# Kernel optimization log

Measured on AMD Instinct MI355X. Metric: run time of the kernel, lower is better.

## Reference

```python
import jax, jax.numpy as jnp
import numpy as np

HID = 256  # LSTM hidden size (hard-coded in Renet)


def _lstm_dir(x, wih, whh, b):
    # x: [N, T, D]; PyTorch LSTM gate order: i, f, g, o
    def cell(carry, xt):
        h, c = carry
        g = xt @ wih.T + h @ whh.T + b
        i, f, gg, o = jnp.split(g, 4, axis=-1)
        c = jax.nn.sigmoid(f) * c + jax.nn.sigmoid(i) * jnp.tanh(gg)
        h = jax.nn.sigmoid(o) * jnp.tanh(c)
        return (h, c), h
    n = x.shape[0]
    h0 = jnp.zeros((n, HID), x.dtype)
    _, hs = jax.lax.scan(cell, (h0, h0), jnp.swapaxes(x, 0, 1))
    return jnp.swapaxes(hs, 0, 1)  # [N, T, HID]


def _bilstm(x, wf, uf, bf, wb, ub, bb):
    hf = _lstm_dir(x, wf, uf, bf)
    hb = _lstm_dir(x[:, ::-1], wb, ub, bb)[:, ::-1]
    return jnp.concatenate([hf, hb], axis=-1)  # [N, T, 2*HID]


def setup_inputs() -> dict:
    key = jax.random.key(0)
    ks = jax.random.split(key, 16)
    B, C, S = 8, 512, 64
    def p(k, shape):
        return 0.05 * jax.random.normal(k, shape, jnp.float32)
    d = {}
    d['x'] = jax.random.normal(ks[0], (B, C, S, S), jnp.float32)
    d['v_wih_f'] = p(ks[1], (4 * HID, C))
    d['v_whh_f'] = p(ks[2], (4 * HID, HID))
    d['v_b_f'] = p(ks[3], (4 * HID,))
    d['v_wih_b'] = p(ks[4], (4 * HID, C))
    d['v_whh_b'] = p(ks[5], (4 * HID, HID))
    d['v_b_b'] = p(ks[6], (4 * HID,))
    d['h_wih_f'] = p(ks[7], (4 * HID, 2 * HID))
    d['h_whh_f'] = p(ks[8], (4 * HID, HID))
    d['h_b_f'] = p(ks[9], (4 * HID,))
    d['h_wih_b'] = p(ks[10], (4 * HID, 2 * HID))
    d['h_whh_b'] = p(ks[11], (4 * HID, HID))
    d['h_b_b'] = p(ks[12], (4 * HID,))
    d['conv_w'] = p(ks[13], (22 * 22, 2 * HID))
    d['conv_b'] = p(ks[14], (22 * 22,))
    return d


def reference(x, v_wih_f, v_whh_f, v_b_f, v_wih_b, v_whh_b, v_b_b,
              h_wih_f, h_whh_f, h_b_f, h_wih_b, h_whh_b, h_b_b,
              conv_w, conv_b):
    B, C, H, W = x.shape
    # ---- Renet ----
    xt = jnp.transpose(x, (0, 2, 3, 1))  # [B,H,W,C]
    # vertical LSTM: sequence along W, batched over all B*H rows at once
    v = _bilstm(xt.reshape(B * H, W, C), v_wih_f, v_whh_f, v_b_f,
                v_wih_b, v_whh_b, v_b_b).reshape(B, H, W, 2 * HID)
    # horizontal LSTM: sequence along H, batched over all B*W columns
    h = _bilstm(jnp.transpose(v, (0, 2, 1, 3)).reshape(B * W, H, 2 * HID),
                h_wih_f, h_whh_f, h_b_f, h_wih_b, h_whh_b,
                h_b_b).reshape(B, W, H, 2 * HID)
    feat = jnp.transpose(h, (0, 3, 2, 1))  # [B, 512, H, W]
    kern = jnp.einsum('bchw,oc->bohw', feat, conv_w) + conv_b[None, :, None, None]
    # ---- PicanetG ----
    kern = jax.nn.softmax(kern, axis=1)  # softmax over 484 channel dim
    # unfold(k=22, dilation=3) with H=W=64 yields exactly one global dilated patch
    patch = x[:, :, ::3, ::3].reshape(B, C, 22 * 22)  # [B, C, 484]
    out = jnp.einsum('bck,bkl->bcl', patch, kern.reshape(B, 22 * 22, H * W))
    return out.reshape(B, C, H, W)
```

## Files before the change

kernel.cpp:

```cpp
#include <hip/hip_runtime.h>
#include <hip/hip_bf16.h>
#include <hip/hip_fp8.h>
#include <math.h>


typedef __hip_bfloat16 bf16;
typedef short short8 __attribute__((ext_vector_type(8)));
typedef float f4 __attribute__((ext_vector_type(4)));
typedef int int4v __attribute__((ext_vector_type(4)));
typedef int int8v __attribute__((ext_vector_type(8)));

#define SCL8 0x7F7F7F7F

__device__ __forceinline__ unsigned short bfbits(float f) {
    bf16 h = __float2bfloat16(f);
    return *reinterpret_cast<unsigned short*>(&h);
}
__device__ __forceinline__ float bf2f(unsigned short u) {
    union { unsigned int i; float f; } x; x.i = ((unsigned int)u) << 16; return x.f;
}
__device__ __forceinline__ unsigned char f2fp8(float f) {
    __hip_fp8_e4m3 q(f);
    return *reinterpret_cast<unsigned char*>(&q);
}
__device__ __forceinline__ float sigm2(float x) {
    return __builtin_amdgcn_rcpf(1.0f + __builtin_amdgcn_exp2f(x * -1.44269504f));
}
__device__ __forceinline__ float tanh2(float x) {
    return 1.0f - 2.0f * __builtin_amdgcn_rcpf(1.0f + __builtin_amdgcn_exp2f(x * 2.88539008f));
}

#define GLD16(g, s) __builtin_amdgcn_global_load_lds(                          \
    (const __attribute__((address_space(1))) void*)(g),                        \
    (__attribute__((address_space(3))) void*)(s), 16, 0, 0)

#define LGKM_BARRIER() do {                                                    \
    asm volatile("s_waitcnt lgkmcnt(0)" ::: "memory");                         \
    __builtin_amdgcn_s_barrier();                                              \
} while (0)

__global__ __launch_bounds__(256)
void prep_weights(const float* __restrict__ w0, const float* __restrict__ w1,
                  const float* __restrict__ w2, const float* __restrict__ w3,
                  const float* __restrict__ cw, const float* __restrict__ cb,
                  const float* __restrict__ u0, const float* __restrict__ u1,
                  const float* __restrict__ u2, const float* __restrict__ u3,
                  bf16* __restrict__ wt, bf16* __restrict__ cw2b,
                  float* __restrict__ cb2, unsigned char* __restrict__ wq)
{
    int idx = blockIdx.x * 256 + threadIdx.x;
    if (idx < 2097152) {
        int mat = idx >> 19, rem = idx & 524287;
        const float* src = (mat == 0) ? w0 : (mat == 1) ? w1 : (mat == 2) ? w2 : w3;
        wt[idx] = __float2bfloat16(src[rem]);
    } else if (idx < 2097152 + 262144) {
        int r = idx - 2097152; int o = r >> 9, k = r & 511;
        cw2b[r] = __float2bfloat16((o < 484) ? cw[o * 512 + k] : 0.f);
    } else if (idx < 2097152 + 262144 + 512) {
        int o = idx - 2097152 - 262144;
        cb2[o] = (o < 484) ? cb[o] : 0.f;
    } else if (idx < 2097152 + 262144 + 512 + 1048576) {
        int r = idx - 2097152 - 262144 - 512;
        int mat = r >> 18, rem = r & 262143;
        const float* src = (mat == 0) ? u0 : (mat == 1) ? u1 : (mat == 2) ? u2 : u3;
        wq[r] = f2fp8(src[rem]);
    }
}

__global__ __launch_bounds__(256)
void xtrans(const float* __restrict__ x, bf16* __restrict__ xt)
{
    __shared__ float T[64][65];
    const int tid = threadIdx.x;
    const int bid = blockIdx.x;
    const int b = bid >> 9, h = (bid >> 3) & 63, ct = bid & 7;
    const int c0 = ct << 6;
    const float* xp = x + ((long)(b * 512 + c0) * 64 + h) * 64;
    const int wv = tid >> 6, wl = tid & 63;
    #pragma unroll
    for (int r = 0; r < 16; ++r) {
        int ci = wv + (r << 2);
        T[ci][wl] = xp[(long)ci * 4096 + wl];
    }
    __syncthreads();
    const int wr = tid >> 2, cj = (tid & 3) << 4;
    bf16* op = xt + ((long)(b * 4096 + h * 64 + wr) * 512) + c0 + cj;
    short8 v0, v1;
    #pragma unroll
    for (int i = 0; i < 8; ++i) v0[i] = (short)bfbits(T[cj + i][wr]);
    #pragma unroll
    for (int i = 0; i < 8; ++i) v1[i] = (short)bfbits(T[cj + 8 + i][wr]);
    *(short8*)op = v0;
    *(short8*)(op + 8) = v1;
}

template<int MODE>
__global__ __launch_bounds__(256)
void gemm_lds(const bf16* __restrict__ A, const bf16* __restrict__ W,
              const float* __restrict__ biasf, const float* __restrict__ biasb,
              void* __restrict__ outf, void* __restrict__ outb, int dironly)
{
    __shared__ alignas(16) char Abuf[16384];
    __shared__ alignas(16) char Bbuf[16384];
    const int tid = threadIdx.x;
    const int wv = tid >> 6, l = tid & 63;
    const int lm = l & 15, lg = l >> 4;
    const int wm = wv >> 1, wn = wv & 1;

    const int nx = gridDim.x;
    int bid = blockIdx.y * nx + blockIdx.x;
    const int cpx = (nx * gridDim.y) >> 3;
    bid = (bid & 7) * cpx + (bid >> 3);
    const int bx = bid % nx;
    const int n0 = (bid / nx) << 7;

    int dir = 0, jblk = 0, g0 = 0;
    const bf16* Wg = W;
    if (MODE == 0) {
        dir  = (dironly < 0) ? (bx >> 3) : dironly;
        jblk = (dironly < 0) ? (bx & 7) : bx;
    } else {
        g0 = bx << 7;
        if (MODE == 2) Wg += (long)(n0 >> 9) * 2097152;
    }

    f4 acc[4][4];
    #pragma unroll
    for (int mf = 0; mf < 4; ++mf)
        #pragma unroll
        for (int nf = 0; nf < 4; ++nf)
            acc[mf][nf] = (f4){0.f, 0.f, 0.f, 0.f};

    for (int kt = 0; kt < 8; ++kt) {
        const int k0 = kt << 6;
        #pragma unroll
        for (int i = 0; i < 4; ++i) {
            const int seg = (wv << 2) + i;
            const int L = (seg << 10) + l * 16;
            const int row = L >> 7;
            const int off = (L & 127) ^ ((row & 7) << 4);
            const bf16* ga = A + (long)(n0 + row) * 512 + k0 + (off >> 1);
            GLD16(ga, &Abuf[seg << 10]);
        }
        #pragma unroll
        for (int i = 0; i < 4; ++i) {
            const int seg = (wv << 2) + i;
            const int L = (seg << 10) + l * 16;
            const int row = L >> 7;
            const int off = (L & 127) ^ ((row & 7) << 4);
            int wrow;
            if (MODE == 0) wrow = (dir << 10) + ((row >> 5) << 8) + jblk * 32 + (row & 31);
            else           wrow = g0 + row;
            const bf16* gb = Wg + (long)wrow * 512 + k0 + (off >> 1);
            GLD16(gb, &Bbuf[seg << 10]);
        }
        __syncthreads();

        #pragma unroll
        for (int kk = 0; kk < 2; ++kk) {
            short8 af[4], bq[4];
            #pragma unroll
            for (int mf = 0; mf < 4; ++mf) {
                const int row = wm * 64 + mf * 16 + lm;
                const int ad = (row << 7) + ((((kk << 6) + (lg << 4))) ^ ((row & 7) << 4));
                af[mf] = *(const short8*)&Abuf[ad];
            }
            #pragma unroll
            for (int nf = 0; nf < 4; ++nf) {
                const int row = (MODE == 0) ? (nf * 32 + wn * 16 + lm)
                                            : (wn * 64 + nf * 16 + lm);
                const int ad = (row << 7) + ((((kk << 6) + (lg << 4))) ^ ((row & 7) << 4));
                bq[nf] = *(const short8*)&Bbuf[ad];
            }
            #pragma unroll
            for (int mf = 0; mf < 4; ++mf)
                #pragma unroll
                for (int nf = 0; nf < 4; ++nf)
                    acc[mf][nf] = __builtin_amdgcn_mfma_f32_16x16x32_bf16(af[mf], bq[nf], acc[mf][nf], 0, 0, 0);
        }
        __syncthreads();
    }

    if (MODE == 0) {
        const float* bs = dir ? biasb : biasf;
        const int jglob = jblk * 32 + wn * 16 + lm;
        float bv[4];
        #pragma unroll
        for (int nf = 0; nf < 4; ++nf) bv[nf] = bs[nf * 256 + jglob];
        ushort4* Gd = (ushort4*)(dir ? outb : outf);
        #pragma unroll
        for (int mf = 0; mf < 4; ++mf) {
            #pragma unroll
            for (int r = 0; r < 4; ++r) {
                const int n = n0 + wm * 64 + mf * 16 + lg * 4 + r;
                ushort4 u;
                u.x = bfbits(acc[mf][0][r] + bv[0]);
                u.y = bfbits(acc[mf][1][r] + bv[1]);
                u.z = bfbits(acc[mf][2][r] + bv[2]);
                u.w = bfbits(acc[mf][3][r] + bv[3]);
                Gd[(long)n * 256 + jglob] = u;
            }
        }
    } else if (MODE == 1) {
        float bv[4];
        #pragma unroll
        for (int nf = 0; nf < 4; ++nf) bv[nf] = biasf[g0 + wn * 64 + nf * 16 + lm];
        float* o = (float*)outf;
        #pragma unroll
        for (int mf = 0; mf < 4; ++mf)
            #pragma unroll
            for (int r = 0; r < 4; ++r) {
                const int n = n0 + wm * 64 + mf * 16 + lg * 4 + r;
                #pragma unroll
                for (int nf = 0; nf < 4; ++nf)
                    o[(long)n * 512 + g0 + wn * 64 + nf * 16 + lm] = acc[mf][nf][r] + bv[nf];
            }
    } else {
        float* o = (float*)outf;
        #pragma unroll
        for (int mf = 0; mf < 4; ++mf)
            #pragma unroll
            for (int r = 0; r < 4; ++r) {
                const int n = n0 + wm * 64 + mf * 16 + lg * 4 + r;
                #pragma unroll
                for (int nf = 0; nf < 4; ++nf)
                    o[(long)n * 4096 + g0 + wn * 64 + nf * 16 + lm] = acc[mf][nf][r];
            }
    }
}

__global__ __launch_bounds__(1024, 4)
void lstm4s(const bf16* __restrict__ Gf, const bf16* __restrict__ Gb,
            const unsigned char* __restrict__ Wqf, const unsigned char* __restrict__ Wqb,
            bf16* __restrict__ Out, int dir_force)
{
    __shared__ char ldspad[83968];
    __shared__ unsigned char hbuf[2][4][256];
    const int tid = threadIdx.x;
    const int wv = tid >> 6, l = tid & 63;
    const int lm = l & 15, lg = l >> 4;
    const int j_c = wv * 16 + lm;
    const int s_a = lm >> 2;

    int dir, sblk;
    if (dir_force >= 0) { dir = dir_force; sblk = blockIdx.x; }
    else               { dir = blockIdx.x >> 7; sblk = blockIdx.x & 127; }
    if (dir_force == -9999) ((volatile char*)ldspad)[tid] = 1;

    const bf16* G = dir ? Gb : Gf;
    const unsigned char* WQ = dir ? Wqb : Wqf;
    const int s0 = sblk << 2;

    int8v wfrag[4][2];
    #pragma unroll
    for (int q = 0; q < 4; ++q) {
        const unsigned char* wr = WQ + (long)(q * 256 + wv * 16 + lm) * 256 + lg * 32;
        #pragma unroll
        for (int kt = 0; kt < 2; ++kt) {
            int4v lo = *(const int4v*)(wr + kt * 128);
            int4v hi = *(const int4v*)(wr + kt * 128 + 16);
            int8v w;
            w[0] = lo[0]; w[1] = lo[1]; w[2] = lo[2]; w[3] = lo[3];
            w[4] = hi[0]; w[5] = hi[1]; w[6] = hi[2]; w[7] = hi[3];
            wfrag[q][kt] = w;
        }
    }

    if (tid < 256) ((unsigned long*)hbuf)[tid] = 0ul;

    float cst = 0.f;
    const ushort4* G4 = (const ushort4*)G;
    const int sg = s0 + lg;
    const long gb0 = (long)sg * 16384 + j_c;
    const long ob0 = ((long)((s0 >> 6) * 4096 + (s0 & 63) + lg)) * 512 + (dir << 8) + j_c;
    unsigned short* Ou = (unsigned short*)Out;

    ushort4 uA, uB;
    {
        int t0 = dir ? 63 : 0, t1 = dir ? 62 : 1;
        uA = G4[gb0 + (long)t0 * 256];
        uB = G4[gb0 + (long)t1 * 256];
    }
    LGKM_BARRIER();

#define LSTM_STEP(SP, UREG, RB, WB)                                             \
    {                                                                           \
        const int t_ = dir ? (63 - (SP)) : (SP);                                \
        \
        int8v af0, af1;                                                         \
        {                                                                       \
            const unsigned char* hb = &hbuf[RB][s_a][0];                        \
            const int c0 = ((lg << 5) + (s_a << 5)) & 255;                      \
            const int c1 = (128 + (lg << 5) + (s_a << 5)) & 255;                \
            int4v a0 = *(const int4v*)(hb + c0);                                \
            int4v a1 = *(const int4v*)(hb + c0 + 16);                           \
            int4v b0 = *(const int4v*)(hb + c1);                                \
            int4v b1 = *(const int4v*)(hb + c1 + 16);                           \
            af0[0]=a0[0]; af0[1]=a0[1]; af0[2]=a0[2]; af0[3]=a0[3];             \
            af0[4]=a1[0]; af0[5]=a1[1]; af0[6]=a1[2]; af0[7]=a1[3];             \
            af1[0]=b0[0]; af1[1]=b0[1]; af1[2]=b0[2]; af1[3]=b0[3];             \
            af1[4]=b1[0]; af1[5]=b1[1]; af1[6]=b1[2]; af1[7]=b1[3];             \
        }                                                                       \
                   \
        f4 ac0 = {0.f,0.f,0.f,0.f}, ac1 = {0.f,0.f,0.f,0.f};                    \
        f4 ac2 = {0.f,0.f,0.f,0.f}, ac3 = {0.f,0.f,0.f,0.f};                    \
        ac0[0] = bf2f(UREG.x); ac1[0] = bf2f(UREG.y);                           \
        ac2[0] = bf2f(UREG.z); ac3[0] = bf2f(UREG.w);                           \
                  \
        {                                                                       \
            int sp2 = (SP) + 2; if (sp2 > 63) sp2 = 63;                         \
            int tp = dir ? (63 - sp2) : sp2;                                    \
            UREG = G4[gb0 + (long)tp * 256];                                    \
        }                                                                       \
        ac0 = __builtin_amdgcn_mfma_scale_f32_16x16x128_f8f6f4(af0, wfrag[0][0], ac0, 0, 0, 0, SCL8, 0, SCL8); \
        ac1 = __builtin_amdgcn_mfma_scale_f32_16x16x128_f8f6f4(af0, wfrag[1][0], ac1, 0, 0, 0, SCL8, 0, SCL8); \
        ac2 = __builtin_amdgcn_mfma_scale_f32_16x16x128_f8f6f4(af0, wfrag[2][0], ac2, 0, 0, 0, SCL8, 0, SCL8); \
        ac3 = __builtin_amdgcn_mfma_scale_f32_16x16x128_f8f6f4(af0, wfrag[3][0], ac3, 0, 0, 0, SCL8, 0, SCL8); \
        ac0 = __builtin_amdgcn_mfma_scale_f32_16x16x128_f8f6f4(af1, wfrag[0][1], ac0, 0, 0, 0, SCL8, 0, SCL8); \
        ac1 = __builtin_amdgcn_mfma_scale_f32_16x16x128_f8f6f4(af1, wfrag[1][1], ac1, 0, 0, 0, SCL8, 0, SCL8); \
        ac2 = __builtin_amdgcn_mfma_scale_f32_16x16x128_f8f6f4(af1, wfrag[2][1], ac2, 0, 0, 0, SCL8, 0, SCL8); \
        ac3 = __builtin_amdgcn_mfma_scale_f32_16x16x128_f8f6f4(af1, wfrag[3][1], ac3, 0, 0, 0, SCL8, 0, SCL8); \
                 \
        {                                                                       \
            float ii = sigm2(ac0[0]);                                           \
            float ff = sigm2(ac1[0]);                                           \
            float gc = tanh2(ac2[0]);                                           \
            float oo = sigm2(ac3[0]);                                           \
            float c  = ff * cst + ii * gc;                                      \
            cst = c;                                                            \
            float h_ = oo * tanh2(c);                                           \
            hbuf[WB][lg][(j_c + (lg << 5)) & 255] = f2fp8(h_);                  \
            Ou[ob0 + (long)t_ * 32768] = bfbits(h_);                            \
        }                                                                       \
        LGKM_BARRIER();                                                         \
    }

    for (int sp = 0; sp < 64; sp += 2) {
        LSTM_STEP(sp,     uA, 0, 1)
        LSTM_STEP(sp + 1, uB, 1, 0)
    }
#undef LSTM_STEP
}

__global__ __launch_bounds__(256)
void softmax_rows(const float* __restrict__ cin, bf16* __restrict__ kout)
{
    const int tid = threadIdx.x;
    const int row = blockIdx.x * 4 + (tid >> 6);
    const int l = tid & 63;
    const float* rp = cin + (long)row * 512 + l * 8;
    float v[8];
    *(float4*)&v[0] = *(const float4*)rp;
    *(float4*)&v[4] = *(const float4*)(rp + 4);
    float m = -3.4e38f;
    #pragma unroll
    for (int i = 0; i < 8; ++i) {
        int o = l * 8 + i;
        if (o < 484) m = fmaxf(m, v[i]);
    }
    #pragma unroll
    for (int d = 1; d < 64; d <<= 1) m = fmaxf(m, __shfl_xor(m, d));
    float e[8], s = 0.f;
    #pragma unroll
    for (int i = 0; i < 8; ++i) {
        int o = l * 8 + i;
        e[i] = (o < 484) ? __expf(v[i] - m) : 0.f;
        s += e[i];
    }
    #pragma unroll
    for (int d = 1; d < 64; d <<= 1) s += __shfl_xor(s, d);
    float inv = 1.f / s;
    short8 st;
    #pragma unroll
    for (int i = 0; i < 8; ++i) st[i] = (short)bfbits(e[i] * inv);
    *(short8*)(kout + (long)row * 512 + l * 8) = st;
}

__global__ __launch_bounds__(256)
void gather_patch(const float* __restrict__ x, bf16* __restrict__ Pch)
{
    int idx = blockIdx.x * 256 + threadIdx.x;
    if (idx >= 2097152) return;
    int o = idx & 511, c = (idx >> 9) & 511, b = idx >> 18;
    float v = 0.f;
    if (o < 484) {
        int i = o / 22, jj = o - i * 22;
        v = x[(long)b * 2097152 + (long)c * 4096 + i * 192 + jj * 3];
    }
    Pch[idx] = __float2bfloat16(v);
}

extern "C" void kernel_launch(void* const* d_in, const int* in_sizes, int n_in,
                              void* d_out, int out_size, void* d_ws, size_t ws_size,
                              hipStream_t stream)
{
    const float* x        = (const float*)d_in[0];
    const float* v_wih_f  = (const float*)d_in[1];
    const float* v_whh_f  = (const float*)d_in[2];
    const float* v_b_f    = (const float*)d_in[3];
    const float* v_wih_b  = (const float*)d_in[4];
    const float* v_whh_b  = (const float*)d_in[5];
    const float* v_b_b    = (const float*)d_in[6];
    const float* h_wih_f  = (const float*)d_in[7];
    const float* h_whh_f  = (const float*)d_in[8];
    const float* h_b_f    = (const float*)d_in[9];
    const float* h_wih_b  = (const float*)d_in[10];
    const float* h_whh_b  = (const float*)d_in[11];
    const float* h_b_b    = (const float*)d_in[12];
    const float* conv_w   = (const float*)d_in[13];
    const float* conv_b   = (const float*)d_in[14];

    const size_t REQ_FUSED  = 50331648UL * 4UL;
    const size_t REQ_SERIAL = 33554432UL * 4UL;
    if (ws_size < REQ_SERIAL) return;
    const bool fused = (ws_size >= REQ_FUSED);

    float* wsf = (float*)d_ws;
    float* out = (float*)d_out;

    bf16*          wt   = (bf16*)(out + 8388608);
    bf16*          cw2b = (bf16*)(out + 9437184);
    float*         cb2  = out + 9568256;
    unsigned char* wq   = (unsigned char*)(out + 9568768);

    prep_weights<<<13314, 256, 0, stream>>>(v_wih_f, v_wih_b, h_wih_f, h_wih_b,
                                            conv_w, conv_b,
                                            v_whh_f, v_whh_b, h_whh_f, h_whh_b,
                                            wt, cw2b, cb2, wq);
    bf16* wt_v = wt;
    bf16* wt_h = wt + 1048576;
    unsigned char* wq_vf = wq;
    unsigned char* wq_vb = wq + 262144;
    unsigned char* wq_hf = wq + 524288;
    unsigned char* wq_hb = wq + 786432;

    dim3 gG(16, 256);
    dim3 gGs(8, 256);
    dim3 gC(4, 256);
    dim3 gF(32, 32);

    if (fused) {
        bf16*  Gf    = (bf16*)d_ws;
        bf16*  Gb    = (bf16*)(wsf + 16777216);
        bf16*  V     = (bf16*)(wsf + 33554432);
        bf16*  HF    = (bf16*)(wsf + 41943040);
        bf16*  xt    = V;
        float* convo = (float*)d_ws;
        bf16*  kernT = Gb;
        bf16*  Pch   = V;

        xtrans<<<4096, 256, 0, stream>>>(x, xt);
        gemm_lds<0><<<gG, 256, 0, stream>>>(xt, wt_v, v_b_f, v_b_b, Gf, Gb, -1);
        lstm4s<<<256, 1024, 0, stream>>>(Gf, Gb, wq_vf, wq_vb, V, -1);

        gemm_lds<0><<<gG, 256, 0, stream>>>(V, wt_h, h_b_f, h_b_b, Gf, Gb, -1);
        lstm4s<<<256, 1024, 0, stream>>>(Gf, Gb, wq_hf, wq_hb, HF, -1);

        gemm_lds<1><<<gC, 256, 0, stream>>>(HF, cw2b, cb2, nullptr, convo, nullptr, 0);
        softmax_rows<<<8192, 256, 0, stream>>>(convo, kernT);
        gather_patch<<<8192, 256, 0, stream>>>(x, Pch);
        gemm_lds<2><<<gF, 256, 0, stream>>>(Pch, kernT, nullptr, nullptr, out, nullptr, 0);
    } else {
        bf16*  G     = (bf16*)d_ws;
        bf16*  V     = (bf16*)(wsf + 16777216);
        bf16*  xt    = (bf16*)(wsf + 25165824);
        bf16*  HF    = xt;
        float* convo = (float*)d_ws;
        bf16*  kernT = V;
        bf16*  Pch   = (bf16*)d_ws;

        xtrans<<<4096, 256, 0, stream>>>(x, xt);
        gemm_lds<0><<<gGs, 256, 0, stream>>>(xt, wt_v, v_b_f, v_b_b, G, G, 0);
        lstm4s<<<128, 1024, 0, stream>>>(G, G, wq_vf, wq_vf, V, 0);
        gemm_lds<0><<<gGs, 256, 0, stream>>>(xt, wt_v, v_b_f, v_b_b, G, G, 1);
        lstm4s<<<128, 1024, 0, stream>>>(G, G, wq_vb, wq_vb, V, 1);

        gemm_lds<0><<<gGs, 256, 0, stream>>>(V, wt_h, h_b_f, h_b_b, G, G, 0);
        lstm4s<<<128, 1024, 0, stream>>>(G, G, wq_hf, wq_hf, HF, 0);
        gemm_lds<0><<<gGs, 256, 0, stream>>>(V, wt_h, h_b_f, h_b_b, G, G, 1);
        lstm4s<<<128, 1024, 0, stream>>>(G, G, wq_hb, wq_hb, HF, 1);

        gemm_lds<1><<<gC, 256, 0, stream>>>(HF, cw2b, cb2, nullptr, convo, nullptr, 0);
        softmax_rows<<<8192, 256, 0, stream>>>(convo, kernT);
        gather_patch<<<8192, 256, 0, stream>>>(x, Pch);
        gemm_lds<2><<<gF, 256, 0, stream>>>(Pch, kernT, nullptr, nullptr, out, nullptr, 0);
    }
}
```

Baseline: 444.8 us.

## Fuse 1x1 conv GEMM with channel softmax into single kernel

```diff
diff --git a/kernel.cpp b/kernel.cpp
--- a/kernel.cpp
+++ b/kernel.cpp
@@ -201,20 +201,6 @@
                 Gd[(long)n * 256 + jglob] = u;
             }
         }
-    } else if (MODE == 1) {
-        float bv[4];
-        #pragma unroll
-        for (int nf = 0; nf < 4; ++nf) bv[nf] = biasf[g0 + wn * 64 + nf * 16 + lm];
-        float* o = (float*)outf;
-        #pragma unroll
-        for (int mf = 0; mf < 4; ++mf)
-            #pragma unroll
-            for (int r = 0; r < 4; ++r) {
-                const int n = n0 + wm * 64 + mf * 16 + lg * 4 + r;
-                #pragma unroll
-                for (int nf = 0; nf < 4; ++nf)
-                    o[(long)n * 512 + g0 + wn * 64 + nf * 16 + lm] = acc[mf][nf][r] + bv[nf];
-            }
     } else {
         float* o = (float*)outf;
         #pragma unroll
@@ -226,6 +212,168 @@
                 for (int nf = 0; nf < 4; ++nf)
                     o[(long)n * 4096 + g0 + wn * 64 + nf * 16 + lm] = acc[mf][nf][r];
             }
+    }
+}
+
+__global__ __launch_bounds__(512)
+void conv_sm(const bf16* __restrict__ A, const bf16* __restrict__ W,
+             const float* __restrict__ bias, bf16* __restrict__ KT)
+{
+    __shared__ alignas(16) char SMEM[83968];
+    char* Ab = SMEM;
+    char* Bb = SMEM + 16384;
+    float (*red)[4] = (float(*)[4])(SMEM + 81920);
+
+    const int tid = threadIdx.x;
+    const int wv = tid >> 6, l = tid & 63;
+    const int lm = l & 15, lg = l >> 4;
+    const int wm = wv >> 2, wn = wv & 3;
+    const int n0 = blockIdx.x << 7;
+
+    f4 acc[4][8];
+    #pragma unroll
+    for (int mf = 0; mf < 4; ++mf)
+        #pragma unroll
+        for (int nf = 0; nf < 8; ++nf)
+            acc[mf][nf] = (f4){0.f, 0.f, 0.f, 0.f};
+
+    for (int kt = 0; kt < 8; ++kt) {
+        const int k0 = kt << 6;
+        #pragma unroll
+        for (int i = 0; i < 2; ++i) {
+            const int L = (i << 13) + tid * 16;
+            const int row = L >> 7;
+            const int off = (L & 127) ^ ((row & 7) << 4);
+            GLD16(A + (long)(n0 + row) * 512 + k0 + (off >> 1),
+                  Ab + (i << 13) + (wv << 10));
+        }
+        #pragma unroll
+        for (int j = 0; j < 8; ++j) {
+            const int L = (j << 13) + tid * 16;
+            const int row = L >> 7;
+            const int off = (L & 127) ^ ((row & 7) << 4);
+            GLD16(W + (long)row * 512 + k0 + (off >> 1),
+                  Bb + (j << 13) + (wv << 10));
+        }
+        __syncthreads();
+        #pragma unroll
+        for (int kk = 0; kk < 2; ++kk) {
+            short8 af[4], bq[8];
+            #pragma unroll
+            for (int mf = 0; mf < 4; ++mf) {
+                const int row = wm * 64 + mf * 16 + lm;
+                const int ad = (row << 7) + ((((kk << 6) + (lg << 4))) ^ ((row & 7) << 4));
+                af[mf] = *(const short8*)&Ab[ad];
+            }
+            #pragma unroll
+            for (int nf = 0; nf < 8; ++nf) {
+                const int row = wn * 128 + nf * 16 + lm;
+                const int ad = (row << 7) + ((((kk << 6) + (lg << 4))) ^ ((row & 7) << 4));
+                bq[nf] = *(const short8*)&Bb[ad];
+            }
+            #pragma unroll
+            for (int mf = 0; mf < 4; ++mf)
+                #pragma unroll
+                for (int nf = 0; nf < 8; ++nf)
+                    acc[mf][nf] = __builtin_amdgcn_mfma_f32_16x16x32_bf16(af[mf], bq[nf], acc[mf][nf], 0, 0, 0);
+        }
+        __syncthreads();
+    }
+
+    float bv[8];
+    bool alive[8];
+    #pragma unroll
+    for (int nf = 0; nf < 8; ++nf) {
+        const int col = wn * 128 + nf * 16 + lm;
+        bv[nf] = bias[col];
+        alive[nf] = (col < 484);
+    }
+
+    #pragma unroll
+    for (int mf = 0; mf < 4; ++mf) {
+        #pragma unroll
+        for (int r = 0; r < 4; ++r) {
+            float m = -3.4e38f;
+            #pragma unroll
+            for (int nf = 0; nf < 8; ++nf) {
+                float v = acc[mf][nf][r] + bv[nf];
+                if (alive[nf]) m = fmaxf(m, v);
+            }
+            m = fmaxf(m, __shfl_xor(m, 1));
+            m = fmaxf(m, __shfl_xor(m, 2));
+            m = fmaxf(m, __shfl_xor(m, 4));
+            m = fmaxf(m, __shfl_xor(m, 8));
+            if (lm == 0) red[wm * 64 + mf * 16 + lg * 4 + r][wn] = m;
+        }
+    }
+    __syncthreads();
+    float mxv[4][4];
+    #pragma unroll
+    for (int mf = 0; mf < 4; ++mf)
+        #pragma unroll
+        for (int r = 0; r < 4; ++r) {
+            const int row = wm * 64 + mf * 16 + lg * 4 + r;
+            mxv[mf][r] = fmaxf(fmaxf(red[row][0], red[row][1]),
+                               fmaxf(red[row][2], red[row][3]));
+        }
+    __syncthreads();
+    #pragma unroll
+    for (int mf = 0; mf < 4; ++mf) {
+        #pragma unroll
+        for (int r = 0; r < 4; ++r) {
+            float s = 0.f;
+            #pragma unroll
+            for (int nf = 0; nf < 8; ++nf) {
+                float v = acc[mf][nf][r] + bv[nf];
+                float e = alive[nf]
+                    ? __builtin_amdgcn_exp2f((v - mxv[mf][r]) * 1.44269504f) : 0.f;
+                acc[mf][nf][r] = e;
+                s += e;
+            }
+            s += __shfl_xor(s, 1);
+            s += __shfl_xor(s, 2);
+            s += __shfl_xor(s, 4);
+            s += __shfl_xor(s, 8);
+            if (lm == 0) red[wm * 64 + mf * 16 + lg * 4 + r][wn] = s;
+        }
+    }
+    __syncthreads();
+    float invv[4][4];
+    #pragma unroll
+    for (int mf = 0; mf < 4; ++mf)
+        #pragma unroll
+        for (int r = 0; r < 4; ++r) {
+            const int row = wm * 64 + mf * 16 + lg * 4 + r;
+            invv[mf][r] = __builtin_amdgcn_rcpf(red[row][0] + red[row][1] +
+                                                red[row][2] + red[row][3]);
+        }
+
+    unsigned short* TB = (unsigned short*)Bb;
+    unsigned short* KTu = (unsigned short*)KT;
+    #pragma unroll
+    for (int hm = 0; hm < 2; ++hm) {
+        __syncthreads();
+        if (wm == hm) {
+            #pragma unroll
+            for (int mf = 0; mf < 4; ++mf)
+                #pragma unroll
+                for (int r = 0; r < 4; ++r) {
+                    const int rr = mf * 16 + lg * 4 + r;
+                    #pragma unroll
+                    for (int nf = 0; nf < 8; ++nf)
+                        TB[rr * 512 + wn * 128 + nf * 16 + lm] =
+                            bfbits(acc[mf][nf][r] * invv[mf][r]);
+                }
+        }
+        __syncthreads();
+        #pragma unroll
+        for (int s = 0; s < 8; ++s) {
+            const int L = (s << 13) + tid * 16;
+            const int rr = L >> 10;
+            const int cc = (L & 1023) >> 1;
+            *(short8*)(KTu + (long)(n0 + hm * 64 + rr) * 512 + cc) =
+                *(const short8*)((const char*)TB + L);
+        }
     }
 }
 
@@ -286,7 +434,6 @@
 #define LSTM_STEP(SP, UREG, RB, WB)                                             \
     {                                                                           \
         const int t_ = dir ? (63 - (SP)) : (SP);                                \
-        \
         int8v af0, af1;                                                         \
         {                                                                       \
             const unsigned char* hb = &hbuf[RB][s_a][0];                        \
@@ -301,12 +448,10 @@
             af1[0]=b0[0]; af1[1]=b0[1]; af1[2]=b0[2]; af1[3]=b0[3];             \
             af1[4]=b1[0]; af1[5]=b1[1]; af1[6]=b1[2]; af1[7]=b1[3];             \
         }                                                                       \
-                   \
         f4 ac0 = {0.f,0.f,0.f,0.f}, ac1 = {0.f,0.f,0.f,0.f};                    \
         f4 ac2 = {0.f,0.f,0.f,0.f}, ac3 = {0.f,0.f,0.f,0.f};                    \
         ac0[0] = bf2f(UREG.x); ac1[0] = bf2f(UREG.y);                           \
         ac2[0] = bf2f(UREG.z); ac3[0] = bf2f(UREG.w);                           \
-                  \
         {                                                                       \
             int sp2 = (SP) + 2; if (sp2 > 63) sp2 = 63;                         \
             int tp = dir ? (63 - sp2) : sp2;                                    \
@@ -320,7 +465,6 @@
         ac1 = __builtin_amdgcn_mfma_scale_f32_16x16x128_f8f6f4(af1, wfrag[1][1], ac1, 0, 0, 0, SCL8, 0, SCL8); \
         ac2 = __builtin_amdgcn_mfma_scale_f32_16x16x128_f8f6f4(af1, wfrag[2][1], ac2, 0, 0, 0, SCL8, 0, SCL8); \
         ac3 = __builtin_amdgcn_mfma_scale_f32_16x16x128_f8f6f4(af1, wfrag[3][1], ac3, 0, 0, 0, SCL8, 0, SCL8); \
-                 \
         {                                                                       \
             float ii = sigm2(ac0[0]);                                           \
             float ff = sigm2(ac1[0]);                                           \
@@ -340,40 +484,6 @@
         LSTM_STEP(sp + 1, uB, 1, 0)
     }
 #undef LSTM_STEP
-}
-
-__global__ __launch_bounds__(256)
-void softmax_rows(const float* __restrict__ cin, bf16* __restrict__ kout)
-{
-    const int tid = threadIdx.x;
-    const int row = blockIdx.x * 4 + (tid >> 6);
-    const int l = tid & 63;
-    const float* rp = cin + (long)row * 512 + l * 8;
-    float v[8];
-    *(float4*)&v[0] = *(const float4*)rp;
-    *(float4*)&v[4] = *(const float4*)(rp + 4);
-    float m = -3.4e38f;
-    #pragma unroll
-    for (int i = 0; i < 8; ++i) {
-        int o = l * 8 + i;
-        if (o < 484) m = fmaxf(m, v[i]);
-    }
-    #pragma unroll
-    for (int d = 1; d < 64; d <<= 1) m = fmaxf(m, __shfl_xor(m, d));
-    float e[8], s = 0.f;
-    #pragma unroll
-    for (int i = 0; i < 8; ++i) {
-        int o = l * 8 + i;
-        e[i] = (o < 484) ? __expf(v[i] - m) : 0.f;
-        s += e[i];
-    }
-    #pragma unroll
-    for (int d = 1; d < 64; d <<= 1) s += __shfl_xor(s, d);
-    float inv = 1.f / s;
-    short8 st;
-    #pragma unroll
-    for (int i = 0; i < 8; ++i) st[i] = (short)bfbits(e[i] * inv);
-    *(short8*)(kout + (long)row * 512 + l * 8) = st;
 }
 
 __global__ __launch_bounds__(256)
@@ -436,7 +546,6 @@
 
     dim3 gG(16, 256);
     dim3 gGs(8, 256);
-    dim3 gC(4, 256);
     dim3 gF(32, 32);
 
     if (fused) {
@@ -445,7 +554,6 @@
         bf16*  V     = (bf16*)(wsf + 33554432);
         bf16*  HF    = (bf16*)(wsf + 41943040);
         bf16*  xt    = V;
-        float* convo = (float*)d_ws;
         bf16*  kernT = Gb;
         bf16*  Pch   = V;
 
@@ -456,8 +564,7 @@
         gemm_lds<0><<<gG, 256, 0, stream>>>(V, wt_h, h_b_f, h_b_b, Gf, Gb, -1);
         lstm4s<<<256, 1024, 0, stream>>>(Gf, Gb, wq_hf, wq_hb, HF, -1);
 
-        gemm_lds<1><<<gC, 256, 0, stream>>>(HF, cw2b, cb2, nullptr, convo, nullptr, 0);
-        softmax_rows<<<8192, 256, 0, stream>>>(convo, kernT);
+        conv_sm<<<256, 512, 0, stream>>>(HF, cw2b, cb2, kernT);
         gather_patch<<<8192, 256, 0, stream>>>(x, Pch);
         gemm_lds<2><<<gF, 256, 0, stream>>>(Pch, kernT, nullptr, nullptr, out, nullptr, 0);
     } else {
@@ -465,7 +572,6 @@
         bf16*  V     = (bf16*)(wsf + 16777216);
         bf16*  xt    = (bf16*)(wsf + 25165824);
         bf16*  HF    = xt;
-        float* convo = (float*)d_ws;
         bf16*  kernT = V;
         bf16*  Pch   = (bf16*)d_ws;
 
@@ -480,8 +586,7 @@
         gemm_lds<0><<<gGs, 256, 0, stream>>>(V, wt_h, h_b_f, h_b_b, G, G, 1);
         lstm4s<<<128, 1024, 0, stream>>>(G, G, wq_hb, wq_hb, HF, 1);
 
-        gemm_lds<1><<<gC, 256, 0, stream>>>(HF, cw2b, cb2, nullptr, convo, nullptr, 0);
-        softmax_rows<<<8192, 256, 0, stream>>>(convo, kernT);
+        conv_sm<<<256, 512, 0, stream>>>(HF, cw2b, cb2, kernT);
         gather_patch<<<8192, 256, 0, stream>>>(x, Pch);
         gemm_lds<2><<<gF, 256, 0, stream>>>(Pch, kernT, nullptr, nullptr, out, nullptr, 0);
     }
```

Result: faster. 427.9 us (-3.8%).
